# Kernel tuning notes

Measured on AMD Instinct MI355X. Metric: run time of the kernel, lower is better.

## Reference

```python
import jax, jax.numpy as jnp
import numpy as np

N_LAYERS = 2
H = 16                      # num_heads
ARW = (1.0, 1.0)            # att_residual_weight
MCB = (0.0, 1.0)            # mask_clip_balancer
LN_EPS = 1e-5


def _ln(x, g, b):
    mu = jnp.mean(x, axis=-1, keepdims=True)
    var = jnp.mean(jnp.square(x - mu), axis=-1, keepdims=True)
    return (x - mu) * jax.lax.rsqrt(var + LN_EPS) * g + b


def _quick_gelu(u):
    return u * jax.nn.sigmoid(1.702 * u)


def setup_inputs() -> dict:
    key = jax.random.key(0)
    ks = jax.random.split(key, 8)
    L, B, C = 577, 8, 1024
    d_ff = 4 * C
    inp = {
        'x': jax.random.normal(ks[0], (L, B, C), jnp.float32),
        'att_bias': jax.random.normal(ks[1], (N_LAYERS, B * H, L, L), jnp.float32),
        'ln1_g': jnp.ones((N_LAYERS, C), jnp.float32),
        'ln1_b': jnp.zeros((N_LAYERS, C), jnp.float32),
        'in_w': 0.02 * jax.random.normal(ks[2], (N_LAYERS, 3 * C, C), jnp.float32),
        'in_b': jnp.zeros((N_LAYERS, 3 * C), jnp.float32),
        'out_w': 0.02 * jax.random.normal(ks[3], (N_LAYERS, C, C), jnp.float32),
        'out_b': jnp.zeros((N_LAYERS, C), jnp.float32),
        'ln2_g': jnp.ones((N_LAYERS, C), jnp.float32),
        'ln2_b': jnp.zeros((N_LAYERS, C), jnp.float32),
        'fc1_w': 0.02 * jax.random.normal(ks[4], (N_LAYERS, d_ff, C), jnp.float32),
        'fc1_b': jnp.zeros((N_LAYERS, d_ff), jnp.float32),
        'fc2_w': 0.02 * jax.random.normal(ks[5], (N_LAYERS, C, d_ff), jnp.float32),
        'fc2_b': jnp.zeros((N_LAYERS, C), jnp.float32),
    }
    return inp


def reference(x, att_bias, ln1_g, ln1_b, in_w, in_b, out_w, out_b,
              ln2_g, ln2_b, fc1_w, fc1_b, fc2_w, fc2_b):
    L, B, C = x.shape
    d = C // H
    scale = d ** -0.5  # custom_att_factor is None
    for i in range(N_LAYERS):
        # --- custom CSA attention ---
        h = _ln(x, ln1_g[i], ln1_b[i])                              # [L,B,C]
        qkv = jnp.einsum('lbc,fc->lbf', h, in_w[i]) + in_b[i]       # [L,B,3C]
        q, k, v = jnp.split(qkv, 3, axis=-1)
        to_heads = lambda t: t.reshape(L, B, H, d).transpose(1, 2, 0, 3)  # [B,H,L,d]
        q, k, v = to_heads(q), to_heads(k), to_heads(v)
        bias = att_bias[i].reshape(B, H, L, L)
        q_attn = bias + scale * jnp.einsum('bhld,bhmd->bhlm', q, q)
        k_attn = bias + scale * jnp.einsum('bhld,bhmd->bhlm', k, k)
        attn = jax.nn.softmax(q_attn, axis=-1) + jax.nn.softmax(k_attn, axis=-1)
        attn = attn * 0.5                                           # norm_att=True
        attn = jnp.mean(attn, axis=1, keepdims=True)                # avg_att=True -> [B,1,L,L]
        out = jnp.matmul(attn, v)                                   # broadcast over H -> [B,H,L,d]
        out = MCB[0] * v + MCB[1] * out
        out = out.transpose(2, 0, 1, 3).reshape(L, B, C)
        out = jnp.einsum('lbc,oc->lbo', out, out_w[i]) + out_b[i]
        x = ARW[0] * x + ARW[1] * out
        # --- MLP residual ---
        h2 = _ln(x, ln2_g[i], ln2_b[i])
        u = _quick_gelu(jnp.einsum('lbc,fc->lbf', h2, fc1_w[i]) + fc1_b[i])
        x = x + jnp.einsum('lbf,cf->lbc', u, fc2_w[i]) + fc2_b[i]
    return x
```

## Files before the change

### kernel.cpp

```cpp
#include <hip/hip_runtime.h>

typedef float f32x4 __attribute__((ext_vector_type(4)));
typedef __bf16 bf16x8 __attribute__((ext_vector_type(8)));

#define L_SEQ 577
#define BB 8
#define CC 1024
#define HH 16
#define ROWS (L_SEQ*BB)

static __device__ __forceinline__ ushort f2b(float f) {
  unsigned u = __float_as_uint(f);
  u += 0x7fffu + ((u >> 16) & 1u);
  return (ushort)(u >> 16);
}

static __device__ __forceinline__ void gld16(const void* g, void* l) {
  __builtin_amdgcn_global_load_lds((const __attribute__((address_space(1))) void*)g,
                                   (__attribute__((address_space(3))) void*)l, 16, 0, 0);
}

__global__ void cvt_kernel(const float* __restrict__ src, ushort* __restrict__ dst, int n4) {
  int i = blockIdx.x * blockDim.x + threadIdx.x;
  if (i < n4) {
    float4 v = *(const float4*)(src + (size_t)i * 4);
    ushort4 o;
    o.x = f2b(v.x); o.y = f2b(v.y); o.z = f2b(v.z); o.w = f2b(v.w);
    *(ushort4*)(dst + (size_t)i * 4) = o;
  }
}

template<int NP, bool DOLN>
__global__ __launch_bounds__(256)
void ln_resid_kernel(const float* __restrict__ xsrc, const float* __restrict__ parts,
                     const float* __restrict__ cbias,
                     const float* __restrict__ g, const float* __restrict__ be,
                     float* __restrict__ xdst, ushort* __restrict__ hout)
{
  const int row = blockIdx.x;
  const int t = threadIdx.x;
  float4 v = *(const float4*)(xsrc + (size_t)row * CC + t * 4);
  if (NP > 0) {
    float4 c4 = *(const float4*)(cbias + t * 4);
    v.x += c4.x; v.y += c4.y; v.z += c4.z; v.w += c4.w;
    #pragma unroll
    for (int p = 0; p < NP; ++p) {
      float4 pv = *(const float4*)(parts + ((size_t)p * ROWS + row) * CC + t * 4);
      v.x += pv.x; v.y += pv.y; v.z += pv.z; v.w += pv.w;
    }
  }
  *(float4*)(xdst + (size_t)row * CC + t * 4) = v;
  if (DOLN) {
    float s  = v.x + v.y + v.z + v.w;
    float s2 = v.x*v.x + v.y*v.y + v.z*v.z + v.w*v.w;
    #pragma unroll
    for (int sd = 1; sd < 64; sd <<= 1) { s += __shfl_xor(s, sd, 64); s2 += __shfl_xor(s2, sd, 64); }
    __shared__ float ps[4], ps2[4];
    const int w = t >> 6;
    if ((t & 63) == 0) { ps[w] = s; ps2[w] = s2; }
    __syncthreads();
    s  = ps[0] + ps[1] + ps[2] + ps[3];
    s2 = ps2[0] + ps2[1] + ps2[2] + ps2[3];
    const float mean = s * (1.f / 1024.f);
    const float var  = s2 * (1.f / 1024.f) - mean * mean;
    const float rstd = rsqrtf(var + 1e-5f);
    float4 gv = *(const float4*)(g + t * 4);
    float4 bv = *(const float4*)(be + t * 4);
    ushort4 o;
    o.x = f2b((v.x - mean) * rstd * gv.x + bv.x);
    o.y = f2b((v.y - mean) * rstd * gv.y + bv.y);
    o.z = f2b((v.z - mean) * rstd * gv.z + bv.z);
    o.w = f2b((v.w - mean) * rstd * gv.w + bv.w);
    *(ushort4*)(hout + (size_t)row * CC + t * 4) = o;
  }
}

__global__ __launch_bounds__(256)
void vt_kernel(const ushort* __restrict__ qkv, ushort* __restrict__ vt)
{
  __shared__ ushort tile[32][33];
  const int lt = blockIdx.x * 32;
  const int nt = blockIdx.y * 32;
  const int b  = blockIdx.z;
  const int tx = threadIdx.x & 31;
  const int ty = threadIdx.x >> 5;
  #pragma unroll
  for (int p = 0; p < 4; ++p) {
    int l = lt + ty + p * 8;
    ushort v = 0;
    if (l < L_SEQ) v = qkv[((size_t)l * BB + b) * 3072 + 2048 + nt + tx];
    tile[ty + p * 8][tx] = v;
  }
  __syncthreads();
  #pragma unroll
  for (int p = 0; p < 4; ++p) {
    int n = nt + ty + p * 8;
    int l = lt + tx;
    vt[((size_t)b * 1024 + n) * 608 + l] = tile[tx][ty + p * 8];
  }
}

__global__ __launch_bounds__(256, 2)
void attn_kernel(const ushort* __restrict__ qkv,
                 const float* __restrict__ bias,
                 float* __restrict__ attnf)
{
  __shared__ float S[2][16][612];
  const int t = threadIdx.x;
  const int lane = t & 63;
  const int w = t >> 6;
  const int rb = blockIdx.x;
  const int b  = blockIdx.y;
  const int hg = blockIdx.z;
  const int r0 = rb * 16;
  float acc[37];
  #pragma unroll
  for (int k = 0; k < 37; ++k) acc[k] = 0.f;

  const int fr = lane & 15;
  const int kc = (lane >> 4) * 8;
  const int arow = min(r0 + fr, L_SEQ - 1);
  const size_t abase = ((size_t)arow * BB + b) * 3072;

  for (int hh = 0; hh < 4; ++hh) {
    const int h = hg * 4 + hh;
    const int qoff = h * 64;
    const int koff = CC + h * 64;
    bf16x8 aq0 = *(const bf16x8*)(qkv + abase + qoff + kc);
    bf16x8 aq1 = *(const bf16x8*)(qkv + abase + qoff + 32 + kc);
    bf16x8 ak0 = *(const bf16x8*)(qkv + abase + koff + kc);
    bf16x8 ak1 = *(const bf16x8*)(qkv + abase + koff + 32 + kc);
    for (int nt = w; nt < 37; nt += 4) {
      const int col = nt * 16 + fr;
      const int ncl = min(col, L_SEQ - 1);
      const size_t brow = ((size_t)ncl * BB + b) * 3072;
      bf16x8 bq0 = *(const bf16x8*)(qkv + brow + qoff + kc);
      bf16x8 bq1 = *(const bf16x8*)(qkv + brow + qoff + 32 + kc);
      bf16x8 bk0 = *(const bf16x8*)(qkv + brow + koff + kc);
      bf16x8 bk1 = *(const bf16x8*)(qkv + brow + koff + 32 + kc);
      f32x4 dq = {0.f, 0.f, 0.f, 0.f};
      f32x4 dk = {0.f, 0.f, 0.f, 0.f};
      dq = __builtin_amdgcn_mfma_f32_16x16x32_bf16(aq0, bq0, dq, 0, 0, 0);
      dq = __builtin_amdgcn_mfma_f32_16x16x32_bf16(aq1, bq1, dq, 0, 0, 0);
      dk = __builtin_amdgcn_mfma_f32_16x16x32_bf16(ak0, bk0, dk, 0, 0, 0);
      dk = __builtin_amdgcn_mfma_f32_16x16x32_bf16(ak1, bk1, dk, 0, 0, 0);
      const bool cvalid = (col < L_SEQ);
      #pragma unroll
      for (int r = 0; r < 4; ++r) {
        int row = (lane >> 4) * 4 + r;
        int l = min(r0 + row, L_SEQ - 1);
        float bs = bias[(((size_t)(b * HH + h)) * L_SEQ + l) * L_SEQ + min(col, L_SEQ - 1)];
        S[0][row][col] = cvalid ? (bs + 0.125f * dq[r]) : -1e30f;
        S[1][row][col] = cvalid ? (bs + 0.125f * dk[r]) : -1e30f;
      }
    }
    __syncthreads();
    const int rr = t >> 4;
    const int j0 = t & 15;
    #pragma unroll
    for (int v = 0; v < 2; ++v) {
      float mx = -1e30f;
      #pragma unroll
      for (int k = 0; k < 37; ++k) mx = fmaxf(mx, S[v][rr][j0 + 16 * k]);
      #pragma unroll
      for (int sd = 1; sd < 16; sd <<= 1) mx = fmaxf(mx, __shfl_xor(mx, sd, 16));
      float e[37]; float sm = 0.f;
      #pragma unroll
      for (int k = 0; k < 37; ++k) { e[k] = __expf(S[v][rr][j0 + 16 * k] - mx); sm += e[k]; }
      #pragma unroll
      for (int sd = 1; sd < 16; sd <<= 1) sm += __shfl_xor(sm, sd, 16);
      float inv = 0.03125f / sm;
      #pragma unroll
      for (int k = 0; k < 37; ++k) acc[k] += e[k] * inv;
    }
    __syncthreads();
  }
  const int rr = t >> 4;
  const int j0 = t & 15;
  const int l = r0 + rr;
  if (l < L_SEQ) {
    float* dst = attnf + (size_t)b * 608 * 608 + (size_t)l * 608;
    #pragma unroll
    for (int k = 0; k < 37; ++k)
      if (j0 + 16 * k < L_SEQ) atomicAdd(dst + j0 + 16 * k, acc[k]);
  }
}

__global__ __launch_bounds__(256, 2)
void av_gemm(const ushort* __restrict__ A, int lda, int Arows, long aStride,
             const ushort* __restrict__ B, int ldb, long bStride,
             int M, int K,
             ushort* __restrict__ outb, int ldo)
{
  __shared__ __align__(16) ushort As[128 * 32];
  __shared__ __align__(16) ushort Bs[128 * 32];
  const int t = threadIdx.x;
  const int lane = t & 63;
  const int w = t >> 6;
  const int bm = blockIdx.x, bn = blockIdx.y, bz = blockIdx.z;
  const ushort* Ab = A + (long)bz * aStride;
  const ushort* Bb = B + (long)bz * bStride;
  const int srow = t >> 2;
  const int sc = (t & 3) * 8;
  const int wr = (w >> 1) * 64;
  const int wc = (w & 1) * 64;
  const int am1 = Arows - 1;
  f32x4 acc[4][4] = {};

  const int r0a = bm * 128 + srow;
  const int r0b = bn * 128 + srow;
  for (int kt = 0; kt < K; kt += 32) {
    __syncthreads();
    gld16(Ab + (size_t)min(r0a, am1) * lda + kt + sc, (void*)(As + t * 8));
    gld16(Ab + (size_t)min(r0a + 64, am1) * lda + kt + sc, (void*)(As + 2048 + t * 8));
    gld16(Bb + (size_t)r0b * ldb + kt + sc, (void*)(Bs + t * 8));
    gld16(Bb + (size_t)(r0b + 64) * ldb + kt + sc, (void*)(Bs + 2048 + t * 8));
    asm volatile("s_waitcnt vmcnt(0)" ::: "memory");
    __syncthreads();
    bf16x8 av[4], bv[4];
    const int fr = lane & 15;
    const int kc = (lane >> 4) * 8;
    #pragma unroll
    for (int m = 0; m < 4; ++m) av[m] = *(const bf16x8*)(As + (wr + m * 16 + fr) * 32 + kc);
    #pragma unroll
    for (int n = 0; n < 4; ++n) bv[n] = *(const bf16x8*)(Bs + (wc + n * 16 + fr) * 32 + kc);
    #pragma unroll
    for (int m = 0; m < 4; ++m)
      #pragma unroll
      for (int n = 0; n < 4; ++n)
        acc[m][n] = __builtin_amdgcn_mfma_f32_16x16x32_bf16(av[m], bv[n], acc[m][n], 0, 0, 0);
  }
  const int rbase = wr + (lane >> 4) * 4;
  const int cbase = wc + (lane & 15);
  #pragma unroll
  for (int n = 0; n < 4; ++n) {
    const int gn = bn * 128 + cbase + n * 16;
    #pragma unroll
    for (int m = 0; m < 4; ++m) {
      f32x4 d = acc[m][n];
      #pragma unroll
      for (int r = 0; r < 4; ++r) {
        const int gm = bm * 128 + rbase + m * 16 + r;
        if (gm < M) outb[((size_t)gm * 8 + bz) * ldo + gn] = f2b(d[r]);
      }
    }
  }
}

#define RD_A8(BOFS, MH) \
  _Pragma("unroll") for (int ks = 0; ks < 2; ++ks) \
  _Pragma("unroll") for (int m = 0; m < 4; ++m) \
    Af[ks][m] = rdA(BOFS, MH, ks, m);

#define RD_B4(BOFS, NH) \
  _Pragma("unroll") for (int ks = 0; ks < 2; ++ks) \
  _Pragma("unroll") for (int n = 0; n < 2; ++n) \
    Bf[NH][ks][n] = rdB(BOFS, NH, ks, n);

#define MFQ(MH, NH) \
  _Pragma("unroll") for (int ks = 0; ks < 2; ++ks) \
  _Pragma("unroll") for (int m = 0; m < 4; ++m) \
  _Pragma("unroll") for (int n = 0; n < 2; ++n) \
    acc[(MH)*4+m][(NH)*2+n] = __builtin_amdgcn_mfma_f32_16x16x32_bf16( \
        Af[ks][m], Bf[NH][ks][n], acc[(MH)*4+m][(NH)*2+n], 0, 0, 0);

#define BARO() \
  __builtin_amdgcn_sched_barrier(0); \
  __builtin_amdgcn_s_barrier(); \
  asm volatile("s_waitcnt lgkmcnt(0)" ::: "memory"); \
  __builtin_amdgcn_sched_barrier(0); \
  __builtin_amdgcn_s_setprio(1);

#define MF_END() \
  __builtin_amdgcn_s_setprio(0); \
  __builtin_amdgcn_sched_barrier(0); \
  __builtin_amdgcn_s_barrier();

template<int EPI>
__global__ __launch_bounds__(512, 2)
void gemm8(const ushort* __restrict__ Ap, int lda, int Arows,
           const ushort* __restrict__ Bp, int ldb,
           int M, int Ksplit,
           const float* __restrict__ bias,
           ushort* __restrict__ outb, float* __restrict__ outf, int ldo)
{
  __shared__ __align__(16) char smem[131072];
  const int t = threadIdx.x;
  const int lane = t & 63;
  const int w = t >> 6;
  const int wm = w >> 2, wn = w & 3;
  const int bm = blockIdx.x, bn = blockIdx.y, bz = blockIdx.z;
  const int k0 = bz * Ksplit;
  const int nkt = Ksplit >> 6;
  const int iters = nkt >> 1;
  const int fr = lane & 15, lq = lane >> 4;

  f32x4 acc[8][4] = {};
  bf16x8 Af[2][4];
  bf16x8 Bf[2][2][2];

  const int rowj0 = t >> 3,        cbj0 = t & 7;
  const int rowj1 = (t + 512) >> 3, cbj1 = (t + 512) & 7;
  const ushort* pA[2][2]; const ushort* pB[2][2];
  #pragma unroll
  for (int h = 0; h < 2; ++h) {
    pA[h][0] = Ap + (size_t)min(bm*256 + h*128 + rowj0, Arows-1) * lda + k0 + ((cbj0 ^ (rowj0 & 7)) << 3);
    pA[h][1] = Ap + (size_t)min(bm*256 + h*128 + rowj1, Arows-1) * lda + k0 + ((cbj1 ^ (rowj1 & 7)) << 3);
    pB[h][0] = Bp + (size_t)(bn*256 + h*128 + rowj0) * ldb + k0 + ((cbj0 ^ (rowj0 & 7)) << 3);
    pB[h][1] = Bp + (size_t)(bn*256 + h*128 + rowj1) * ldb + k0 + ((cbj1 ^ (rowj1 & 7)) << 3);
  }

  auto stA = [&](int kt, int bofs, int h) {
    gld16(pA[h][0] + kt * 64, smem + bofs + h * 16384 + t * 16);
    gld16(pA[h][1] + kt * 64, smem + bofs + h * 16384 + (t + 512) * 16);
  };
  auto stB = [&](int kt, int bofs, int h) {
    gld16(pB[h][0] + kt * 64, smem + bofs + 32768 + h * 16384 + t * 16);
    gld16(pB[h][1] + kt * 64, smem + bofs + 32768 + h * 16384 + (t + 512) * 16);
  };
  auto rdA = [&](int bofs, int mh, int ks, int m) -> bf16x8 {
    const int rl = wm * 64 + m * 16 + fr;
    const int cb = (ks * 4 + lq) ^ (fr & 7);
    return *(const bf16x8*)(smem + bofs + mh * 16384 + rl * 128 + cb * 16);
  };
  auto rdB = [&](int bofs, int nh, int ks, int n) -> bf16x8 {
    const int rl = wn * 32 + n * 16 + fr;
    const int cb = (ks * 4 + lq) ^ (fr & 7);
    return *(const bf16x8*)(smem + bofs + 32768 + nh * 16384 + rl * 128 + cb * 16);
  };

  stA(0, 0, 0); stB(0, 0, 0); stB(0, 0, 1); stA(0, 0, 1);
  stA(1, 65536, 0); stB(1, 65536, 1); stA(1, 65536, 1);
  asm volatile("s_waitcnt vmcnt(6)" ::: "memory");
  __builtin_amdgcn_sched_barrier(0);
  __builtin_amdgcn_s_barrier();

  for (int i = 0; i < iters; ++i) {
    const bool more = (i + 1 < iters);
    const int kt2 = 2 * i + 2;
    RD_A8(0, 0) RD_B4(0, 0)
    stB(2 * i + 1, 65536, 0);
    BARO(); MFQ(0, 0) MF_END();
    RD_B4(0, 1)
    if (more) stA(kt2, 0, 0);
    BARO(); MFQ(0, 1) MF_END();
    RD_A8(0, 1)
    if (more) stB(kt2, 0, 1);
    BARO(); MFQ(1, 1) MF_END();
    if (more) stA(kt2, 0, 1);
    BARO(); MFQ(1, 0)
    __builtin_amdgcn_s_setprio(0);
    if (more) { asm volatile("s_waitcnt vmcnt(6)" ::: "memory"); }
    else      { asm volatile("s_waitcnt vmcnt(0)" ::: "memory"); }
    __builtin_amdgcn_sched_barrier(0);
    __builtin_amdgcn_s_barrier();
    RD_A8(65536, 0) RD_B4(65536, 0)
    if (more) stB(kt2, 0, 0);
    BARO(); MFQ(0, 0) MF_END();
    RD_B4(65536, 1)
    if (more) stA(2 * i + 3, 65536, 0);
    BARO(); MFQ(0, 1) MF_END();
    RD_A8(65536, 1)
    if (more) stB(2 * i + 3, 65536, 1);
    BARO(); MFQ(1, 1) MF_END();
    if (more) stA(2 * i + 3, 65536, 1);
    BARO(); MFQ(1, 0)
    __builtin_amdgcn_s_setprio(0);
    if (more) { asm volatile("s_waitcnt vmcnt(6)" ::: "memory"); }
    __builtin_amdgcn_sched_barrier(0);
    __builtin_amdgcn_s_barrier();
  }

  #pragma unroll
  for (int mh = 0; mh < 2; ++mh)
  #pragma unroll
  for (int nh = 0; nh < 2; ++nh)
  #pragma unroll
  for (int n = 0; n < 2; ++n) {
    const int gn = bn * 256 + nh * 128 + wn * 32 + n * 16 + fr;
    const float bval = (EPI == 4) ? 0.f : bias[gn];
    #pragma unroll
    for (int m = 0; m < 4; ++m) {
      f32x4 d = acc[mh * 4 + m][nh * 2 + n];
      #pragma unroll
      for (int r = 0; r < 4; ++r) {
        const int gm = bm * 256 + mh * 128 + wm * 64 + m * 16 + lq * 4 + r;
        if (gm < M) {
          if (EPI == 0) {
            outb[(size_t)gm * ldo + gn] = f2b(d[r] + bval);
          } else if (EPI == 1) {
            float v0 = d[r] + bval;
            outb[(size_t)gm * ldo + gn] = f2b(v0 / (1.f + __expf(-1.702f * v0)));
          } else {
            outf[((size_t)bz * M + gm) * ldo + gn] = d[r];
          }
        }
      }
    }
  }
}

extern "C" void kernel_launch(void* const* d_in, const int* in_sizes, int n_in,
                              void* d_out, int out_size, void* d_ws, size_t ws_size,
                              hipStream_t stream)
{
  (void)in_sizes; (void)n_in; (void)out_size; (void)ws_size;
  const float* x_in  = (const float*)d_in[0];
  const float* attb  = (const float*)d_in[1];
  const float* ln1_g = (const float*)d_in[2];
  const float* ln1_b = (const float*)d_in[3];
  const float* in_w  = (const float*)d_in[4];
  const float* in_b  = (const float*)d_in[5];
  const float* out_w = (const float*)d_in[6];
  const float* out_b = (const float*)d_in[7];
  const float* ln2_g = (const float*)d_in[8];
  const float* ln2_b = (const float*)d_in[9];
  const float* fc1_w = (const float*)d_in[10];
  const float* fc1_b = (const float*)d_in[11];
  const float* fc2_w = (const float*)d_in[12];
  const float* fc2_b = (const float*)d_in[13];
  float* x = (float*)d_out;

  char* ws = (char*)d_ws;
  size_t off = 0;
  auto alloc = [&](size_t bytes) -> void* {
    void* p = ws + off; off += (bytes + 255) & ~(size_t)255; return p;
  };
  ushort* wIn   = (ushort*)alloc(2ull * 3072 * 1024 * 2);
  ushort* wOut  = (ushort*)alloc(2ull * 1024 * 1024 * 2);
  ushort* wF1   = (ushort*)alloc(2ull * 4096 * 1024 * 2);
  ushort* wF2   = (ushort*)alloc(2ull * 4096 * 1024 * 2);
  ushort* hbuf  = (ushort*)alloc((size_t)ROWS * 1024 * 2);
  ushort* qkv   = (ushort*)alloc((size_t)ROWS * 3072 * 2);
  ushort* vt    = (ushort*)alloc((size_t)8 * 1024 * 608 * 2);
  ushort* attn  = (ushort*)alloc((size_t)8 * 608 * 608 * 2);
  float*  attnf = (float*)alloc((size_t)8 * 608 * 608 * 4);
  ushort* outlb = (ushort*)alloc((size_t)ROWS * 1024 * 2);
  float*  pbuf  = (float*)alloc((size_t)4 * ROWS * 1024 * 4);
  ushort* ubuf  = qkv;

  cvt_kernel<<<2 * 3072 * 1024 / 4 / 256, 256, 0, stream>>>(in_w,  wIn,  2 * 3072 * 1024 / 4);
  cvt_kernel<<<2 * 1024 * 1024 / 4 / 256, 256, 0, stream>>>(out_w, wOut, 2 * 1024 * 1024 / 4);
  cvt_kernel<<<2 * 4096 * 1024 / 4 / 256, 256, 0, stream>>>(fc1_w, wF1,  2 * 4096 * 1024 / 4);
  cvt_kernel<<<2 * 4096 * 1024 / 4 / 256, 256, 0, stream>>>(fc2_w, wF2,  2 * 4096 * 1024 / 4);
  ln_resid_kernel<0, true><<<ROWS, 256, 0, stream>>>(x_in, nullptr, nullptr,
      ln1_g, ln1_b, x, hbuf);

  for (int i = 0; i < 2; ++i) {
    gemm8<0><<<dim3(19, 12, 1), 512, 0, stream>>>(hbuf, 1024, ROWS,
        wIn + (size_t)i * 3072 * 1024, 1024,
        ROWS, 1024, in_b + i * 3072, qkv, nullptr, 3072);
    hipMemsetAsync(attnf, 0, (size_t)8 * 608 * 608 * 4, stream);
    attn_kernel<<<dim3(37, 8, 4), 256, 0, stream>>>(qkv, attb + (size_t)i * 128 * 577 * 577, attnf);
    vt_kernel<<<dim3(19, 32, 8), 256, 0, stream>>>(qkv, vt);
    cvt_kernel<<<8 * 608 * 608 / 4 / 256, 256, 0, stream>>>(attnf, attn, 8 * 608 * 608 / 4);
    av_gemm<<<dim3(5, 8, 8), 256, 0, stream>>>(attn, 608, 577, (long)608 * 608,
        vt, 608, (long)1024 * 608, 577, 608, outlb, 1024);
    gemm8<4><<<dim3(19, 4, 2), 512, 0, stream>>>(outlb, 1024, ROWS,
        wOut + (size_t)i * 1024 * 1024, 1024,
        ROWS, 512, nullptr, nullptr, pbuf, 1024);
    ln_resid_kernel<2, true><<<ROWS, 256, 0, stream>>>(x, pbuf, out_b + i * 1024,
        ln2_g + i * 1024, ln2_b + i * 1024, x, hbuf);
    gemm8<1><<<dim3(19, 16, 1), 512, 0, stream>>>(hbuf, 1024, ROWS,
        wF1 + (size_t)i * 4096 * 1024, 1024,
        ROWS, 1024, fc1_b + i * 4096, ubuf, nullptr, 4096);
    gemm8<4><<<dim3(19, 4, 4), 512, 0, stream>>>(ubuf, 4096, ROWS,
        wF2 + (size_t)i * 4096 * 1024, 4096,
        ROWS, 1024, nullptr, nullptr, pbuf, 1024);
    if (i == 0) {
      ln_resid_kernel<4, true><<<ROWS, 256, 0, stream>>>(x, pbuf, fc2_b,
          ln1_g + 1024, ln1_b + 1024, x, hbuf);
    } else {
      ln_resid_kernel<4, false><<<ROWS, 256, 0, stream>>>(x, pbuf, fc2_b + 1024,
          nullptr, nullptr, x, nullptr);
    }
  }
}
```

Measured before the change: 1.030 ms.

## Prefetch attention operands, replace atomics with partial buffers, remap GEMM tiles per XCD

The attention kernel now software-prefetches the next column tile's Q/K fragments and bias values in registers, and hoists the bias row pointers. Instead of fp32 atomicAdd into a zeroed buffer, each head group writes bf16 partials that a new combine kernel sums, which also removes the memset and the separate convert. The GEMM maps workgroup IDs so neighbouring tiles land on the same XCD for L2 reuse. The four weight-conversion launches are merged into one. Partials are stored in bf16 before summation, which adds a small rounding step.

```diff
diff --git a/kernel.cpp b/kernel.cpp
--- a/kernel.cpp
+++ b/kernel.cpp
@@ -20,14 +20,22 @@
                                    (__attribute__((address_space(3))) void*)l, 16, 0, 0);
 }
 
-__global__ void cvt_kernel(const float* __restrict__ src, ushort* __restrict__ dst, int n4) {
+__global__ void cvt4_kernel(const float* __restrict__ s0, ushort* __restrict__ d0, int n0,
+                            const float* __restrict__ s1, ushort* __restrict__ d1, int n1,
+                            const float* __restrict__ s2, ushort* __restrict__ d2, int n2,
+                            const float* __restrict__ s3, ushort* __restrict__ d3, int n3)
+{
   int i = blockIdx.x * blockDim.x + threadIdx.x;
-  if (i < n4) {
-    float4 v = *(const float4*)(src + (size_t)i * 4);
-    ushort4 o;
-    o.x = f2b(v.x); o.y = f2b(v.y); o.z = f2b(v.z); o.w = f2b(v.w);
-    *(ushort4*)(dst + (size_t)i * 4) = o;
-  }
+  const float* src; ushort* dst;
+  if (i < n0)                { src = s0; dst = d0; }
+  else if ((i -= n0) < n1)   { src = s1; dst = d1; }
+  else if ((i -= n1) < n2)   { src = s2; dst = d2; }
+  else if ((i -= n2) < n3)   { src = s3; dst = d3; }
+  else return;
+  float4 v = *(const float4*)(src + (size_t)i * 4);
+  ushort4 o;
+  o.x = f2b(v.x); o.y = f2b(v.y); o.z = f2b(v.z); o.w = f2b(v.w);
+  *(ushort4*)(dst + (size_t)i * 4) = o;
 }
 
 template<int NP, bool DOLN>
@@ -103,7 +111,7 @@
 __global__ __launch_bounds__(256, 2)
 void attn_kernel(const ushort* __restrict__ qkv,
                  const float* __restrict__ bias,
-                 float* __restrict__ attnf)
+                 ushort* __restrict__ attnp)
 {
   __shared__ float S[2][16][612];
   const int t = threadIdx.x;
@@ -118,7 +126,8 @@
   for (int k = 0; k < 37; ++k) acc[k] = 0.f;
 
   const int fr = lane & 15;
-  const int kc = (lane >> 4) * 8;
+  const int lq = lane >> 4;
+  const int kc = lq * 8;
   const int arow = min(r0 + fr, L_SEQ - 1);
   const size_t abase = ((size_t)arow * BB + b) * 3072;
 
@@ -130,28 +139,53 @@
     bf16x8 aq1 = *(const bf16x8*)(qkv + abase + qoff + 32 + kc);
     bf16x8 ak0 = *(const bf16x8*)(qkv + abase + koff + kc);
     bf16x8 ak1 = *(const bf16x8*)(qkv + abase + koff + 32 + kc);
+    const float* bprow[4];
+    #pragma unroll
+    for (int r = 0; r < 4; ++r) {
+      const int l = min(r0 + lq * 4 + r, L_SEQ - 1);
+      bprow[r] = bias + (((size_t)(b * HH + h)) * L_SEQ + l) * L_SEQ;
+    }
+    bf16x8 nq0, nq1, nk0, nk1;
+    float nbs[4];
+    {
+      const int ncl = min(w * 16 + fr, L_SEQ - 1);
+      const size_t brow = ((size_t)ncl * BB + b) * 3072;
+      nq0 = *(const bf16x8*)(qkv + brow + qoff + kc);
+      nq1 = *(const bf16x8*)(qkv + brow + qoff + 32 + kc);
+      nk0 = *(const bf16x8*)(qkv + brow + koff + kc);
+      nk1 = *(const bf16x8*)(qkv + brow + koff + 32 + kc);
+      #pragma unroll
+      for (int r = 0; r < 4; ++r) nbs[r] = bprow[r][ncl];
+    }
     for (int nt = w; nt < 37; nt += 4) {
-      const int col = nt * 16 + fr;
-      const int ncl = min(col, L_SEQ - 1);
-      const size_t brow = ((size_t)ncl * BB + b) * 3072;
-      bf16x8 bq0 = *(const bf16x8*)(qkv + brow + qoff + kc);
-      bf16x8 bq1 = *(const bf16x8*)(qkv + brow + qoff + 32 + kc);
-      bf16x8 bk0 = *(const bf16x8*)(qkv + brow + koff + kc);
-      bf16x8 bk1 = *(const bf16x8*)(qkv + brow + koff + 32 + kc);
+      bf16x8 cq0 = nq0, cq1 = nq1, ck0 = nk0, ck1 = nk1;
+      float cbs[4];
+      #pragma unroll
+      for (int r = 0; r < 4; ++r) cbs[r] = nbs[r];
+      const int nxt = nt + 4;
+      if (nxt < 37) {
+        const int ncl = min(nxt * 16 + fr, L_SEQ - 1);
+        const size_t brow = ((size_t)ncl * BB + b) * 3072;
+        nq0 = *(const bf16x8*)(qkv + brow + qoff + kc);
+        nq1 = *(const bf16x8*)(qkv + brow + qoff + 32 + kc);
+        nk0 = *(const bf16x8*)(qkv + brow + koff + kc);
+        nk1 = *(const bf16x8*)(qkv + brow + koff + 32 + kc);
+        #pragma unroll
+        for (int r = 0; r < 4; ++r) nbs[r] = bprow[r][ncl];
+      }
       f32x4 dq = {0.f, 0.f, 0.f, 0.f};
       f32x4 dk = {0.f, 0.f, 0.f, 0.f};
-      dq = __builtin_amdgcn_mfma_f32_16x16x32_bf16(aq0, bq0, dq, 0, 0, 0);
-      dq = __builtin_amdgcn_mfma_f32_16x16x32_bf16(aq1, bq1, dq, 0, 0, 0);
-      dk = __builtin_amdgcn_mfma_f32_16x16x32_bf16(ak0, bk0, dk, 0, 0, 0);
-      dk = __builtin_amdgcn_mfma_f32_16x16x32_bf16(ak1, bk1, dk, 0, 0, 0);
+      dq = __builtin_amdgcn_mfma_f32_16x16x32_bf16(aq0, cq0, dq, 0, 0, 0);
+      dq = __builtin_amdgcn_mfma_f32_16x16x32_bf16(aq1, cq1, dq, 0, 0, 0);
+      dk = __builtin_amdgcn_mfma_f32_16x16x32_bf16(ak0, ck0, dk, 0, 0, 0);
+      dk = __builtin_amdgcn_mfma_f32_16x16x32_bf16(ak1, ck1, dk, 0, 0, 0);
+      const int col = nt * 16 + fr;
       const bool cvalid = (col < L_SEQ);
       #pragma unroll
       for (int r = 0; r < 4; ++r) {
-        int row = (lane >> 4) * 4 + r;
-        int l = min(r0 + row, L_SEQ - 1);
-        float bs = bias[(((size_t)(b * HH + h)) * L_SEQ + l) * L_SEQ + min(col, L_SEQ - 1)];
-        S[0][row][col] = cvalid ? (bs + 0.125f * dq[r]) : -1e30f;
-        S[1][row][col] = cvalid ? (bs + 0.125f * dk[r]) : -1e30f;
+        const int row = lq * 4 + r;
+        S[0][row][col] = cvalid ? (cbs[r] + 0.125f * dq[r]) : -1e30f;
+        S[1][row][col] = cvalid ? (cbs[r] + 0.125f * dk[r]) : -1e30f;
       }
     }
     __syncthreads();
@@ -179,11 +213,38 @@
   const int j0 = t & 15;
   const int l = r0 + rr;
   if (l < L_SEQ) {
-    float* dst = attnf + (size_t)b * 608 * 608 + (size_t)l * 608;
-    #pragma unroll
-    for (int k = 0; k < 37; ++k)
-      if (j0 + 16 * k < L_SEQ) atomicAdd(dst + j0 + 16 * k, acc[k]);
-  }
+    ushort* dstp = attnp + ((size_t)hg * 8 + b) * 608 * 608 + (size_t)l * 608;
+    #pragma unroll
+    for (int k = 0; k < 37; ++k) dstp[j0 + 16 * k] = f2b(acc[k]);
+  }
+}
+
+__global__ __launch_bounds__(256)
+void attn_combine(const ushort* __restrict__ attnp, ushort* __restrict__ attn)
+{
+  const int t = threadIdx.x;
+  if (t >= 152) return;
+  const int l = blockIdx.x;
+  const int b = blockIdx.y;
+  const int c0 = t * 4;
+  const size_t base = ((size_t)b * 608 + l) * 608 + c0;
+  const size_t hs = (size_t)8 * 608 * 608;
+  float s[4] = {0.f, 0.f, 0.f, 0.f};
+  #pragma unroll
+  for (int p = 0; p < 4; ++p) {
+    ushort4 v = *(const ushort4*)(attnp + p * hs + base);
+    s[0] += __uint_as_float((unsigned)v.x << 16);
+    s[1] += __uint_as_float((unsigned)v.y << 16);
+    s[2] += __uint_as_float((unsigned)v.z << 16);
+    s[3] += __uint_as_float((unsigned)v.w << 16);
+  }
+  ushort4 o;
+  const bool lv = (l < L_SEQ);
+  o.x = (lv && c0 + 0 < L_SEQ) ? f2b(s[0]) : (ushort)0;
+  o.y = (lv && c0 + 1 < L_SEQ) ? f2b(s[1]) : (ushort)0;
+  o.z = (lv && c0 + 2 < L_SEQ) ? f2b(s[2]) : (ushort)0;
+  o.w = (lv && c0 + 3 < L_SEQ) ? f2b(s[3]) : (ushort)0;
+  *(ushort4*)(attn + base) = o;
 }
 
 __global__ __launch_bounds__(256, 2)
@@ -289,10 +350,18 @@
   const int lane = t & 63;
   const int w = t >> 6;
   const int wm = w >> 2, wn = w & 3;
-  const int bm = blockIdx.x, bn = blockIdx.y, bz = blockIdx.z;
+  const int gx = gridDim.x;
+  const int nwg = gx * gridDim.y;
+  int id = blockIdx.y * gx + blockIdx.x;
+  {
+    const int q8 = nwg >> 3, r8 = nwg & 7;
+    const int xcd = id & 7, pos = id >> 3;
+    id = (xcd < r8 ? xcd * (q8 + 1) : r8 * (q8 + 1) + (xcd - r8) * q8) + pos;
+  }
+  const int bm = id % gx, bn = id / gx;
+  const int bz = blockIdx.z;
   const int k0 = bz * Ksplit;
-  const int nkt = Ksplit >> 6;
-  const int iters = nkt >> 1;
+  const int iters = Ksplit >> 7;
   const int fr = lane & 15, lq = lane >> 4;
 
   f32x4 acc[8][4] = {};
@@ -434,15 +503,16 @@
   ushort* qkv   = (ushort*)alloc((size_t)ROWS * 3072 * 2);
   ushort* vt    = (ushort*)alloc((size_t)8 * 1024 * 608 * 2);
   ushort* attn  = (ushort*)alloc((size_t)8 * 608 * 608 * 2);
-  float*  attnf = (float*)alloc((size_t)8 * 608 * 608 * 4);
+  ushort* attnp = (ushort*)alloc((size_t)4 * 8 * 608 * 608 * 2);
   ushort* outlb = (ushort*)alloc((size_t)ROWS * 1024 * 2);
   float*  pbuf  = (float*)alloc((size_t)4 * ROWS * 1024 * 4);
   ushort* ubuf  = qkv;
 
-  cvt_kernel<<<2 * 3072 * 1024 / 4 / 256, 256, 0, stream>>>(in_w,  wIn,  2 * 3072 * 1024 / 4);
-  cvt_kernel<<<2 * 1024 * 1024 / 4 / 256, 256, 0, stream>>>(out_w, wOut, 2 * 1024 * 1024 / 4);
-  cvt_kernel<<<2 * 4096 * 1024 / 4 / 256, 256, 0, stream>>>(fc1_w, wF1,  2 * 4096 * 1024 / 4);
-  cvt_kernel<<<2 * 4096 * 1024 / 4 / 256, 256, 0, stream>>>(fc2_w, wF2,  2 * 4096 * 1024 / 4);
+  cvt4_kernel<<<(1572864 + 524288 + 2097152 + 2097152 + 255) / 256, 256, 0, stream>>>(
+      in_w,  wIn,  1572864,
+      out_w, wOut, 524288,
+      fc1_w, wF1,  2097152,
+      fc2_w, wF2,  2097152);
   ln_resid_kernel<0, true><<<ROWS, 256, 0, stream>>>(x_in, nullptr, nullptr,
       ln1_g, ln1_b, x, hbuf);
 
@@ -450,10 +520,9 @@
     gemm8<0><<<dim3(19, 12, 1), 512, 0, stream>>>(hbuf, 1024, ROWS,
         wIn + (size_t)i * 3072 * 1024, 1024,
         ROWS, 1024, in_b + i * 3072, qkv, nullptr, 3072);
-    hipMemsetAsync(attnf, 0, (size_t)8 * 608 * 608 * 4, stream);
-    attn_kernel<<<dim3(37, 8, 4), 256, 0, stream>>>(qkv, attb + (size_t)i * 128 * 577 * 577, attnf);
+    attn_kernel<<<dim3(37, 8, 4), 256, 0, stream>>>(qkv, attb + (size_t)i * 128 * 577 * 577, attnp);
     vt_kernel<<<dim3(19, 32, 8), 256, 0, stream>>>(qkv, vt);
-    cvt_kernel<<<8 * 608 * 608 / 4 / 256, 256, 0, stream>>>(attnf, attn, 8 * 608 * 608 / 4);
+    attn_combine<<<dim3(608, 8), 256, 0, stream>>>(attnp, attn);
     av_gemm<<<dim3(5, 8, 8), 256, 0, stream>>>(attn, 608, 577, (long)608 * 608,
         vt, 608, (long)1024 * 608, 577, 608, outlb, 1024);
     gemm8<4><<<dim3(19, 4, 2), 512, 0, stream>>>(outlb, 1024, ROWS,
```

Result: faster. 975.1 us (-5.3%).
